# Kernel tuning notes

Measured on AMD Instinct MI355X. Metric: run time of the kernel, lower is better.

## Reference

```python
import jax, jax.numpy as jnp
import numpy as np

ALPHA_LO = float(np.exp(-1.0 / 5.0))   # 0.8187
ALPHA_HI = float(np.exp(-1.0 / 25.0))  # 0.9608
BN_EPS = 1e-5

B, T, D_IN, H = 32, 2000, 512, 512


def setup_inputs() -> dict:
    key = jax.random.key(0)
    ks = jax.random.split(key, 5)
    x = jax.random.normal(ks[0], (B, T, D_IN), dtype=jnp.float32)
    W = jax.random.normal(ks[1], (H, D_IN), dtype=jnp.float32) / np.sqrt(D_IN)
    b = jax.random.normal(ks[2], (H,), dtype=jnp.float32) * 0.01
    alpha = jax.random.uniform(ks[3], (H,), dtype=jnp.float32,
                               minval=ALPHA_LO, maxval=ALPHA_HI)
    gamma = jnp.ones((H,), dtype=jnp.float32)
    beta = jnp.zeros((H,), dtype=jnp.float32)
    ut0 = jax.random.uniform(ks[4], (B, H), dtype=jnp.float32)
    return {"x": x, "W": W, "b": b, "alpha": alpha,
            "gamma": gamma, "beta": beta, "ut0": ut0}


def reference(x, W, b, alpha, gamma, beta, ut0):
    # Linear: [B,T,Din] @ [Din,H] + b
    Wx = jnp.einsum("btd,hd->bth", x, W) + b
    # BatchNorm1d (training forward): stats over flattened (B*T) dim
    flat = Wx.reshape(-1, Wx.shape[-1])
    mean = flat.mean(axis=0)
    var = flat.var(axis=0)  # biased, as torch BN uses for normalization
    Wx = ((flat - mean) * jax.lax.rsqrt(var + BN_EPS) * gamma + beta).reshape(Wx.shape)
    # Readout cell: leaky integration + softmax accumulation over time
    a = jnp.clip(alpha, ALPHA_LO, ALPHA_HI)

    def step(carry, wxt):
        ut, acc = carry
        ut = a * ut + (1.0 - a) * wxt          # [B,H]
        acc = acc + jax.nn.softmax(ut, axis=1)
        return (ut, acc), None

    wx_t = jnp.transpose(Wx, (1, 0, 2))  # [T,B,H]
    (_, out), _ = jax.lax.scan(step, (ut0, jnp.zeros_like(ut0)), wx_t)
    return out[:, None, :]  # [B,1,H]
```

## Files before the change

### kernel.cpp

```cpp
#include <hip/hip_runtime.h>
#include <hip/hip_bf16.h>
#include <stdint.h>


namespace {
constexpr int kB = 32;
constexpr int kT = 2000;
constexpr int kD = 512;
constexpr int kH = 512;
constexpr int kM = kB * kT;
constexpr int kBM = 64;
constexpr int kNB = kM / kBM;
constexpr int kL = 16;
constexpr int kC = kT / kL;
constexpr int kG = 5;
constexpr int kNG = kC / kG;
constexpr float kALo = 0.81873075307798182f;
constexpr float kAHi = 0.96078943915232320f;

typedef __bf16 bf16x4 __attribute__((ext_vector_type(4)));
typedef __bf16 bf16x8 __attribute__((ext_vector_type(8)));
typedef float floatx16 __attribute__((ext_vector_type(16)));

__device__ __forceinline__ float bf2f(unsigned short u) {
  return __builtin_bit_cast(float, (unsigned)u << 16);
}
__device__ __forceinline__ float clipa(float a) {
  return fminf(fmaxf(a, kALo), kAHi);
}
__device__ __forceinline__ float pow16(float a) {
  const float a2 = a * a, a4 = a2 * a2, a8 = a4 * a4;
  return a8 * a8;
}

__global__ __launch_bounds__(256) void wcvt_k(const float* __restrict__ W,
                                              __bf16* __restrict__ Wbf,
                                              float* __restrict__ sums,
                                              float* __restrict__ out) {
  const int t = blockIdx.x * 256 + threadIdx.x;
  if (t < 2 * kH) sums[t] = 0.f;
  if (t < kB * kH) out[t] = 0.f;
  const float4 a0 = ((const float4*)W)[t * 2];
  const float4 a1 = ((const float4*)W)[t * 2 + 1];
  bf16x8 v;
  v[0] = (__bf16)a0.x; v[1] = (__bf16)a0.y; v[2] = (__bf16)a0.z; v[3] = (__bf16)a0.w;
  v[4] = (__bf16)a1.x; v[5] = (__bf16)a1.y; v[6] = (__bf16)a1.z; v[7] = (__bf16)a1.w;
  const int h = t >> 6, k8 = t & 63;
  *(bf16x8*)(Wbf + ((size_t)k8 * 512 + h) * 8) = v;
}

__global__ __launch_bounds__(512, 4) void gemm_k(const float* __restrict__ X,
                                                 const __bf16* __restrict__ Wbf,
                                                 const float* __restrict__ alpha,
                                                 unsigned short* __restrict__ Wxb,
                                                 float* __restrict__ vbuf,
                                                 float* __restrict__ partial) {
  __shared__ alignas(16) __bf16 As2[2][4][65][8];
  __shared__ float sred[2][kH];
  const int tid = threadIdx.x;
  const size_t row0 = (size_t)blockIdx.x * kBM;
  const int w = tid >> 6, L = tid & 63;
  const int ct0 = w * 2;
  const int lhalf = L >> 5, l32 = L & 31;
  const int arow = tid >> 3, acol = (tid & 7) * 4;
  const int akq = acol >> 3, aoff = acol & 7;

  floatx16 acc[2][2] = {};
  const float* xptr = X + (row0 + arow) * kD + acol;
  const __bf16* bptr = Wbf + ((size_t)(ct0 * 32) + l32) * 8;

  bf16x8 bE[4], bO[4];
  auto loadB = [&](bf16x8* dst, int s) {
#pragma unroll
    for (int kh = 0; kh < 2; ++kh) {
      const int kq = kh * 2 + lhalf;
      const __bf16* bq = bptr + (size_t)(s * 4 + kq) * 4096;
      dst[kh * 2 + 0] = *(const bf16x8*)bq;
      dst[kh * 2 + 1] = *(const bf16x8*)(bq + 256);
    }
  };
  auto stage = [&](int bufIdx, const float4& a) {
    bf16x4 av;
    av[0] = (__bf16)a.x; av[1] = (__bf16)a.y;
    av[2] = (__bf16)a.z; av[3] = (__bf16)a.w;
    *(bf16x4*)&As2[bufIdx][akq][arow][aoff] = av;
  };
  auto computeR = [&](int bufIdx, const bf16x8* bb) {
#pragma unroll
    for (int kh = 0; kh < 2; ++kh) {
      const int kq = kh * 2 + lhalf;
      const bf16x8 af0 = *(const bf16x8*)&As2[bufIdx][kq][l32][0];
      const bf16x8 af1 = *(const bf16x8*)&As2[bufIdx][kq][32 + l32][0];
      acc[0][0] = __builtin_amdgcn_mfma_f32_32x32x16_bf16(af0, bb[kh * 2 + 0], acc[0][0], 0, 0, 0);
      acc[0][1] = __builtin_amdgcn_mfma_f32_32x32x16_bf16(af0, bb[kh * 2 + 1], acc[0][1], 0, 0, 0);
      acc[1][0] = __builtin_amdgcn_mfma_f32_32x32x16_bf16(af1, bb[kh * 2 + 0], acc[1][0], 0, 0, 0);
      acc[1][1] = __builtin_amdgcn_mfma_f32_32x32x16_bf16(af1, bb[kh * 2 + 1], acc[1][1], 0, 0, 0);
    }
  };

  loadB(bE, 0);
  {
    const float4 a0 = *(const float4*)xptr;
    stage(0, a0);
  }
  float4 aA = *(const float4*)(xptr + 1 * 32);
  float4 aB = *(const float4*)(xptr + 2 * 32);
  asm volatile("s_waitcnt lgkmcnt(0)" ::: "memory");
  __builtin_amdgcn_s_barrier();

#pragma unroll 1
  for (int s = 0; s < 16; s += 2) {
    loadB(bO, s + 1);
    stage(1, aA);
    if (s + 3 < 16) aA = *(const float4*)(xptr + (s + 3) * 32);
    computeR(0, bE);
    asm volatile("s_waitcnt lgkmcnt(0)" ::: "memory");
    __builtin_amdgcn_s_barrier();
    const int o = s + 1;
    if (o < 15) {
      loadB(bE, o + 1);
      stage(0, aB);
      if (o + 3 < 16) aB = *(const float4*)(xptr + (o + 3) * 32);
    }
    computeR(1, bO);
    if (o < 15) {
      asm volatile("s_waitcnt lgkmcnt(0)" ::: "memory");
      __builtin_amdgcn_s_barrier();
    }
  }

  __syncthreads();
  sred[0][tid] = 0.f;
  sred[1][tid] = 0.f;
  __syncthreads();
#pragma unroll
  for (int c = 0; c < 2; ++c) {
    float s = 0.f, q = 0.f;
#pragma unroll
    for (int rt = 0; rt < 2; ++rt) {
#pragma unroll
      for (int r = 0; r < 16; ++r) {
        const float v = acc[rt][c][r];
        s += v;
        q += v * v;
      }
    }
    s += __shfl_xor(s, 32);
    q += __shfl_xor(q, 32);
    if (lhalf == 0) {
      atomicAdd(&sred[0][(ct0 + c) * 32 + l32], s);
      atomicAdd(&sred[1][(ct0 + c) * 32 + l32], q);
    }
  }

#pragma unroll
  for (int c = 0; c < 2; ++c) {
    const int col = (ct0 + c) * 32 + l32;
    const float a = clipa(alpha[col]);
    const float oma = 1.0f - a;
    const float a2 = a * a, a4 = a2 * a2, a8 = a4 * a4;
    float wgt[8];
    wgt[0] = a8 * a2 * a; wgt[1] = a8 * a2; wgt[2] = a8 * a; wgt[3] = a8;
    wgt[4] = a2 * a;      wgt[5] = a2;      wgt[6] = a;      wgt[7] = 1.0f;
    const float mult = (lhalf == 0) ? a4 * oma : oma;
#pragma unroll
    for (int j = 0; j < 8; ++j) wgt[j] *= mult;
#pragma unroll
    for (int rt = 0; rt < 2; ++rt) {
#pragma unroll
      for (int c32 = 0; c32 < 2; ++c32) {
        float S = 0.f;
#pragma unroll
        for (int j = 0; j < 8; ++j) S += wgt[j] * acc[rt][c][c32 * 8 + j];
        S += __shfl_xor(S, 32);
        if (lhalf == 0) {
          const int g = (int)blockIdx.x * 4 + rt * 2 + c32;
          vbuf[(size_t)g * kH + col] = S;
        }
      }
    }
  }

#pragma unroll
  for (int rt = 0; rt < 2; ++rt) {
#pragma unroll
    for (int c = 0; c < 2; ++c) {
      const int col = (ct0 + c) * 32 + l32;
#pragma unroll
      for (int r = 0; r < 16; ++r) {
        const int row = rt * 32 + 4 * lhalf + (r & 3) + 8 * (r >> 2);
        const unsigned short u = __builtin_bit_cast(unsigned short, (__bf16)acc[rt][c][r]);
        const unsigned un = __shfl_down((unsigned)u, 1);
        if ((l32 & 1) == 0)
          *(unsigned*)(Wxb + (row0 + row) * (size_t)kH + col) = (unsigned)u | (un << 16);
      }
    }
  }
  __syncthreads();
  partial[(size_t)blockIdx.x * 1024 + tid] = sred[0][tid];
  partial[(size_t)blockIdx.x * 1024 + 512 + tid] = sred[1][tid];
}

__global__ __launch_bounds__(512) void red1_k(const float* __restrict__ partial,
                                              float* __restrict__ sums) {
  const int tid = threadIdx.x;
  const int r0 = blockIdx.x * 25;
  float s0 = 0.f, s1 = 0.f;
#pragma unroll 5
  for (int r = 0; r < 25; ++r) {
    s0 += partial[(size_t)(r0 + r) * 1024 + tid];
    s1 += partial[(size_t)(r0 + r) * 1024 + 512 + tid];
  }
  atomicAdd(&sums[tid], s0);
  atomicAdd(&sums[kH + tid], s1);
}

__global__ __launch_bounds__(512) void fin_scan_k(const float* __restrict__ sums,
                                                  const float* __restrict__ alpha,
                                                  const float* __restrict__ gamma,
                                                  const float* __restrict__ beta,
                                                  const float* __restrict__ ut0,
                                                  float* __restrict__ prm,
                                                  const float* __restrict__ vbuf,
                                                  float* __restrict__ ustart) {
  const int h = threadIdx.x;
  const int b = blockIdx.x;
  const float inv_n = 1.0f / (float)kM;
  const float mean = sums[h] * inv_n;
  const float var = sums[kH + h] * inv_n - mean * mean;
  const float sc = gamma[h] * rsqrtf(var + 1e-5f);
  const float sh = beta[h] - mean * sc;
  const float a = clipa(alpha[h]);
  if (b == 0) {
    prm[h] = sc;
    prm[kH + h] = sh;
    prm[2 * kH + h] = a;
    prm[3 * kH + h] = 1.0f - a;
  }
  const float a16 = pow16(a);
  const float shc = sh * (1.0f - a16);
  float u = ut0[(size_t)b * kH + h];
  float vc[kG];
#pragma unroll 1
  for (int cb = 0; cb < kC; cb += kG) {
#pragma unroll
    for (int j = 0; j < kG; ++j)
      vc[j] = vbuf[((size_t)b * kC + cb + j) * kH + h];
    ustart[((size_t)b * kNG + cb / kG) * kH + h] = u;
#pragma unroll
    for (int j = 0; j < kG; ++j) u = a16 * u + sc * vc[j] + shc;
  }
}

__global__ __launch_bounds__(512) void soft_k(const unsigned short* __restrict__ Wxb,
                                              const float* __restrict__ prm,
                                              const float* __restrict__ ustart,
                                              float* __restrict__ out) {
  __shared__ float part[kL][9];
  __shared__ float zinv[kL];
  const int bc = blockIdx.x;
  const int b = bc / kNG, grp = bc % kNG;
  const int h = threadIdx.x;
  const int wv = h >> 6, lane = h & 63;
  const float sc = prm[h], sh = prm[kH + h];
  const float a = prm[2 * kH + h], oma = prm[3 * kH + h];
  float u = ustart[(size_t)bc * kH + h];
  const unsigned short* base =
      Wxb + ((size_t)b * kT + (size_t)grp * kG * kL) * kH + h;
  float acc = 0.f;
#pragma unroll 1
  for (int cc = 0; cc < kG; ++cc) {
    float e[kL];
#pragma unroll
    for (int i = 0; i < kL; ++i) {
      const float wvx = bf2f(base[(size_t)(cc * kL + i) * kH]) * sc + sh;
      u = a * u + oma * wvx;
      e[i] = __expf(u);
    }
#pragma unroll
    for (int i = 0; i < kL; ++i) {
      float s = e[i];
#pragma unroll
      for (int off = 32; off > 0; off >>= 1) s += __shfl_xor(s, off);
      if (lane == 0) part[i][wv] = s;
    }
    __syncthreads();
    if (h < kL) {
      float s = 0.f;
#pragma unroll
      for (int j = 0; j < 8; ++j) s += part[h][j];
      zinv[h] = 1.0f / s;
    }
    __syncthreads();
#pragma unroll
    for (int i = 0; i < kL; ++i) acc += e[i] * zinv[i];
    __syncthreads();
  }
  atomicAdd(&out[(size_t)b * kH + h], acc);
}

}

extern "C" void kernel_launch(void* const* d_in, const int* in_sizes, int n_in,
                              void* d_out, int out_size, void* d_ws, size_t ws_size,
                              hipStream_t stream) {
  const float* x = (const float*)d_in[0];
  const float* Wm = (const float*)d_in[1];
  const float* alpha = (const float*)d_in[3];
  const float* gamma = (const float*)d_in[4];
  const float* beta = (const float*)d_in[5];
  const float* ut0 = (const float*)d_in[6];
  float* out = (float*)d_out;

  float* wsp = (float*)d_ws;
  float* vbuf = wsp;
  float* ustart = vbuf + (size_t)kB * kC * kH;
  float* partial = ustart + (size_t)kB * kNG * kH;
  float* sums = partial + (size_t)1000 * 1024;
  float* prm = sums + 2 * kH;
  __bf16* Wbf = (__bf16*)(prm + 4 * kH);
  unsigned short* Wxb = (unsigned short*)(Wbf + (size_t)kH * kD);

  wcvt_k<<<128, 256, 0, stream>>>(Wm, Wbf, sums, out);
  gemm_k<<<kNB, 512, 0, stream>>>(x, Wbf, alpha, Wxb, vbuf, partial);
  red1_k<<<40, 512, 0, stream>>>(partial, sums);
  fin_scan_k<<<kB, 512, 0, stream>>>(sums, alpha, gamma, beta, ut0, prm, vbuf, ustart);
  soft_k<<<kB * kNG, 512, 0, stream>>>(Wxb, prm, ustart, out);
}
```

Baseline: 302.9 us.

## Load GEMM A operand directly from global into registers, drop LDS staging

The GEMM kernel no longer stages X tiles through shared memory with barriers. Each lane now loads its own MFMA A-fragment rows straight from global memory into registers, double-buffered, and converts them to bf16 in place. This removes the LDS writes, the LDS reads and the per-step barriers. In exchange every wave redundantly reads the same X rows (8 waves share the 64-row tile), and register use rises, so the occupancy hint is lowered from 4 to 2 blocks per CU.

Result: slower. 387.3 us (+27.9%).

```diff
diff --git a/kernel.cpp b/kernel.cpp
--- a/kernel.cpp
+++ b/kernel.cpp
@@ -49,27 +49,39 @@
   *(bf16x8*)(Wbf + ((size_t)k8 * 512 + h) * 8) = v;
 }
 
-__global__ __launch_bounds__(512, 4) void gemm_k(const float* __restrict__ X,
+__global__ __launch_bounds__(512, 2) void gemm_k(const float* __restrict__ X,
                                                  const __bf16* __restrict__ Wbf,
                                                  const float* __restrict__ alpha,
                                                  unsigned short* __restrict__ Wxb,
                                                  float* __restrict__ vbuf,
                                                  float* __restrict__ partial) {
-  __shared__ alignas(16) __bf16 As2[2][4][65][8];
   __shared__ float sred[2][kH];
   const int tid = threadIdx.x;
   const size_t row0 = (size_t)blockIdx.x * kBM;
   const int w = tid >> 6, L = tid & 63;
   const int ct0 = w * 2;
   const int lhalf = L >> 5, l32 = L & 31;
-  const int arow = tid >> 3, acol = (tid & 7) * 4;
-  const int akq = acol >> 3, aoff = acol & 7;
 
   floatx16 acc[2][2] = {};
-  const float* xptr = X + (row0 + arow) * kD + acol;
+  const float* xr0 = X + (row0 + l32) * kD + lhalf * 8;
+  const float* xr1 = X + (row0 + 32 + l32) * kD + lhalf * 8;
   const __bf16* bptr = Wbf + ((size_t)(ct0 * 32) + l32) * 8;
 
+  float4 aE[4][2], aO[4][2];
   bf16x8 bE[4], bO[4];
+
+  auto loadA = [&](float4 (*dst)[2], int s) {
+#pragma unroll
+    for (int rt = 0; rt < 2; ++rt) {
+      const float* xr = rt ? xr1 : xr0;
+#pragma unroll
+      for (int kh = 0; kh < 2; ++kh) {
+        const float* p = xr + s * 32 + kh * 16;
+        dst[rt * 2 + kh][0] = *(const float4*)p;
+        dst[rt * 2 + kh][1] = *(const float4*)(p + 4);
+      }
+    }
+  };
   auto loadB = [&](bf16x8* dst, int s) {
 #pragma unroll
     for (int kh = 0; kh < 2; ++kh) {
@@ -79,53 +91,47 @@
       dst[kh * 2 + 1] = *(const bf16x8*)(bq + 256);
     }
   };
-  auto stage = [&](int bufIdx, const float4& a) {
-    bf16x4 av;
-    av[0] = (__bf16)a.x; av[1] = (__bf16)a.y;
-    av[2] = (__bf16)a.z; av[3] = (__bf16)a.w;
-    *(bf16x4*)&As2[bufIdx][akq][arow][aoff] = av;
+  auto cvt8 = [](const float4 (&f)[2]) {
+    bf16x8 v;
+    v[0] = (__bf16)f[0].x; v[1] = (__bf16)f[0].y;
+    v[2] = (__bf16)f[0].z; v[3] = (__bf16)f[0].w;
+    v[4] = (__bf16)f[1].x; v[5] = (__bf16)f[1].y;
+    v[6] = (__bf16)f[1].z; v[7] = (__bf16)f[1].w;
+    return v;
   };
-  auto computeR = [&](int bufIdx, const bf16x8* bb) {
-#pragma unroll
-    for (int kh = 0; kh < 2; ++kh) {
-      const int kq = kh * 2 + lhalf;
-      const bf16x8 af0 = *(const bf16x8*)&As2[bufIdx][kq][l32][0];
-      const bf16x8 af1 = *(const bf16x8*)&As2[bufIdx][kq][32 + l32][0];
-      acc[0][0] = __builtin_amdgcn_mfma_f32_32x32x16_bf16(af0, bb[kh * 2 + 0], acc[0][0], 0, 0, 0);
-      acc[0][1] = __builtin_amdgcn_mfma_f32_32x32x16_bf16(af0, bb[kh * 2 + 1], acc[0][1], 0, 0, 0);
-      acc[1][0] = __builtin_amdgcn_mfma_f32_32x32x16_bf16(af1, bb[kh * 2 + 0], acc[1][0], 0, 0, 0);
-      acc[1][1] = __builtin_amdgcn_mfma_f32_32x32x16_bf16(af1, bb[kh * 2 + 1], acc[1][1], 0, 0, 0);
-    }
-  };
-
-  loadB(bE, 0);
-  {
-    const float4 a0 = *(const float4*)xptr;
-    stage(0, a0);
-  }
-  float4 aA = *(const float4*)(xptr + 1 * 32);
-  float4 aB = *(const float4*)(xptr + 2 * 32);
-  asm volatile("s_waitcnt lgkmcnt(0)" ::: "memory");
-  __builtin_amdgcn_s_barrier();
+
+  loadA(aE, 0); loadB(bE, 0);
+  loadA(aO, 1); loadB(bO, 1);
 
 #pragma unroll 1
   for (int s = 0; s < 16; s += 2) {
-    loadB(bO, s + 1);
-    stage(1, aA);
-    if (s + 3 < 16) aA = *(const float4*)(xptr + (s + 3) * 32);
-    computeR(0, bE);
-    asm volatile("s_waitcnt lgkmcnt(0)" ::: "memory");
-    __builtin_amdgcn_s_barrier();
-    const int o = s + 1;
-    if (o < 15) {
-      loadB(bE, o + 1);
-      stage(0, aB);
-      if (o + 3 < 16) aB = *(const float4*)(xptr + (o + 3) * 32);
-    }
-    computeR(1, bO);
-    if (o < 15) {
-      asm volatile("s_waitcnt lgkmcnt(0)" ::: "memory");
-      __builtin_amdgcn_s_barrier();
+    {
+      bf16x8 af[4];
+#pragma unroll
+      for (int f = 0; f < 4; ++f) af[f] = cvt8(aE[f]);
+      if (s + 2 < 16) loadA(aE, s + 2);
+#pragma unroll
+      for (int kh = 0; kh < 2; ++kh) {
+        acc[0][0] = __builtin_amdgcn_mfma_f32_32x32x16_bf16(af[kh], bE[kh * 2 + 0], acc[0][0], 0, 0, 0);
+        acc[0][1] = __builtin_amdgcn_mfma_f32_32x32x16_bf16(af[kh], bE[kh * 2 + 1], acc[0][1], 0, 0, 0);
+        acc[1][0] = __builtin_amdgcn_mfma_f32_32x32x16_bf16(af[2 + kh], bE[kh * 2 + 0], acc[1][0], 0, 0, 0);
+        acc[1][1] = __builtin_amdgcn_mfma_f32_32x32x16_bf16(af[2 + kh], bE[kh * 2 + 1], acc[1][1], 0, 0, 0);
+      }
+      if (s + 2 < 16) loadB(bE, s + 2);
+    }
+    {
+      bf16x8 af[4];
+#pragma unroll
+      for (int f = 0; f < 4; ++f) af[f] = cvt8(aO[f]);
+      if (s + 3 < 16) loadA(aO, s + 3);
+#pragma unroll
+      for (int kh = 0; kh < 2; ++kh) {
+        acc[0][0] = __builtin_amdgcn_mfma_f32_32x32x16_bf16(af[kh], bO[kh * 2 + 0], acc[0][0], 0, 0, 0);
+        acc[0][1] = __builtin_amdgcn_mfma_f32_32x32x16_bf16(af[kh], bO[kh * 2 + 1], acc[0][1], 0, 0, 0);
+        acc[1][0] = __builtin_amdgcn_mfma_f32_32x32x16_bf16(af[2 + kh], bO[kh * 2 + 0], acc[1][0], 0, 0, 0);
+        acc[1][1] = __builtin_amdgcn_mfma_f32_32x32x16_bf16(af[2 + kh], bO[kh * 2 + 1], acc[1][1], 0, 0, 0);
+      }
+      if (s + 3 < 16) loadB(bO, s + 3);
     }
   }
 
```

## Restructure softmax pass to one wave per 16-step chunk with in-wave reductions

Applied to the files above, without the earlier changes.

The scan kernel now writes the carried state at every 16-step chunk boundary in place into vbuf, instead of every 80 steps into a separate ustart buffer. The softmax kernel assigns one 64-lane wave per (batch, chunk), with each lane covering 8 hidden units loaded as a vector. The softmax normalizer is therefore a pure wave shuffle reduction with no shared memory or block barriers, and the grid grows to 1000 blocks for more parallelism. The GEMM block index is also swizzled so neighbouring blocks cover distant row tiles, which changes L2/channel access patterns. Per-element atomics to out increase in number.

Result: slower. 332.2 us (+9.7%).

```diff
diff --git a/kernel.cpp b/kernel.cpp
--- a/kernel.cpp
+++ b/kernel.cpp
@@ -14,12 +14,12 @@
 constexpr int kL = 16;
 constexpr int kC = kT / kL;
 constexpr int kG = 5;
-constexpr int kNG = kC / kG;
 constexpr float kALo = 0.81873075307798182f;
 constexpr float kAHi = 0.96078943915232320f;
 
 typedef __bf16 bf16x4 __attribute__((ext_vector_type(4)));
 typedef __bf16 bf16x8 __attribute__((ext_vector_type(8)));
+typedef unsigned short u16x8 __attribute__((ext_vector_type(8)));
 typedef float floatx16 __attribute__((ext_vector_type(16)));
 
 __device__ __forceinline__ float bf2f(unsigned short u) {
@@ -58,7 +58,8 @@
   __shared__ alignas(16) __bf16 As2[2][4][65][8];
   __shared__ float sred[2][kH];
   const int tid = threadIdx.x;
-  const size_t row0 = (size_t)blockIdx.x * kBM;
+  const int swz = (blockIdx.x & 7) * (kNB / 8) + (blockIdx.x >> 3);
+  const size_t row0 = (size_t)swz * kBM;
   const int w = tid >> 6, L = tid & 63;
   const int ct0 = w * 2;
   const int lhalf = L >> 5, l32 = L & 31;
@@ -174,7 +175,7 @@
         for (int j = 0; j < 8; ++j) S += wgt[j] * acc[rt][c][c32 * 8 + j];
         S += __shfl_xor(S, 32);
         if (lhalf == 0) {
-          const int g = (int)blockIdx.x * 4 + rt * 2 + c32;
+          const int g = swz * 4 + rt * 2 + c32;
           vbuf[(size_t)g * kH + col] = S;
         }
       }
@@ -221,8 +222,7 @@
                                                   const float* __restrict__ beta,
                                                   const float* __restrict__ ut0,
                                                   float* __restrict__ prm,
-                                                  const float* __restrict__ vbuf,
-                                                  float* __restrict__ ustart) {
+                                                  float* __restrict__ vbuf) {
   const int h = threadIdx.x;
   const int b = blockIdx.x;
   const float inv_n = 1.0f / (float)kM;
@@ -246,57 +246,61 @@
 #pragma unroll
     for (int j = 0; j < kG; ++j)
       vc[j] = vbuf[((size_t)b * kC + cb + j) * kH + h];
-    ustart[((size_t)b * kNG + cb / kG) * kH + h] = u;
-#pragma unroll
-    for (int j = 0; j < kG; ++j) u = a16 * u + sc * vc[j] + shc;
-  }
-}
-
-__global__ __launch_bounds__(512) void soft_k(const unsigned short* __restrict__ Wxb,
-                                              const float* __restrict__ prm,
-                                              const float* __restrict__ ustart,
-                                              float* __restrict__ out) {
-  __shared__ float part[kL][9];
-  __shared__ float zinv[kL];
-  const int bc = blockIdx.x;
-  const int b = bc / kNG, grp = bc % kNG;
-  const int h = threadIdx.x;
-  const int wv = h >> 6, lane = h & 63;
-  const float sc = prm[h], sh = prm[kH + h];
-  const float a = prm[2 * kH + h], oma = prm[3 * kH + h];
-  float u = ustart[(size_t)bc * kH + h];
-  const unsigned short* base =
-      Wxb + ((size_t)b * kT + (size_t)grp * kG * kL) * kH + h;
-  float acc = 0.f;
-#pragma unroll 1
-  for (int cc = 0; cc < kG; ++cc) {
-    float e[kL];
-#pragma unroll
-    for (int i = 0; i < kL; ++i) {
-      const float wvx = bf2f(base[(size_t)(cc * kL + i) * kH]) * sc + sh;
-      u = a * u + oma * wvx;
-      e[i] = __expf(u);
-    }
-#pragma unroll
-    for (int i = 0; i < kL; ++i) {
-      float s = e[i];
-#pragma unroll
-      for (int off = 32; off > 0; off >>= 1) s += __shfl_xor(s, off);
-      if (lane == 0) part[i][wv] = s;
-    }
-    __syncthreads();
-    if (h < kL) {
-      float s = 0.f;
-#pragma unroll
-      for (int j = 0; j < 8; ++j) s += part[h][j];
-      zinv[h] = 1.0f / s;
-    }
-    __syncthreads();
-#pragma unroll
-    for (int i = 0; i < kL; ++i) acc += e[i] * zinv[i];
-    __syncthreads();
-  }
-  atomicAdd(&out[(size_t)b * kH + h], acc);
+#pragma unroll
+    for (int j = 0; j < kG; ++j) {
+      vbuf[((size_t)b * kC + cb + j) * kH + h] = u;
+      u = a16 * u + sc * vc[j] + shc;
+    }
+  }
+}
+
+__global__ __launch_bounds__(256, 4) void soft_k(const unsigned short* __restrict__ Wxb,
+                                                 const float* __restrict__ prm,
+                                                 const float* __restrict__ ustart,
+                                                 float* __restrict__ out) {
+  const int tid = threadIdx.x;
+  const int wv = tid >> 6, lane = tid & 63;
+  const int unit = blockIdx.x * 4 + wv;
+  const int b = unit / kC, c = unit % kC;
+  const int h0 = lane * 8;
+
+  float sc[8], sh[8], av[8], om[8], u[8], acc[8];
+  *(float4*)&sc[0] = *(const float4*)(prm + h0);
+  *(float4*)&sc[4] = *(const float4*)(prm + h0 + 4);
+  *(float4*)&sh[0] = *(const float4*)(prm + kH + h0);
+  *(float4*)&sh[4] = *(const float4*)(prm + kH + h0 + 4);
+  *(float4*)&av[0] = *(const float4*)(prm + 2 * kH + h0);
+  *(float4*)&av[4] = *(const float4*)(prm + 2 * kH + h0 + 4);
+  *(float4*)&om[0] = *(const float4*)(prm + 3 * kH + h0);
+  *(float4*)&om[4] = *(const float4*)(prm + 3 * kH + h0 + 4);
+  const float* up = ustart + ((size_t)b * kC + c) * kH + h0;
+  *(float4*)&u[0] = *(const float4*)up;
+  *(float4*)&u[4] = *(const float4*)(up + 4);
+#pragma unroll
+  for (int j = 0; j < 8; ++j) acc[j] = 0.f;
+
+  const unsigned short* base = Wxb + ((size_t)b * kT + (size_t)c * kL) * kH + h0;
+#pragma unroll
+  for (int i = 0; i < kL; ++i) {
+    const u16x8 v = *(const u16x8*)(base + (size_t)i * kH);
+    float e[8];
+    float ls = 0.f;
+#pragma unroll
+    for (int j = 0; j < 8; ++j) {
+      const float wvx = bf2f(v[j]) * sc[j] + sh[j];
+      u[j] = av[j] * u[j] + om[j] * wvx;
+      e[j] = __expf(u[j]);
+      ls += e[j];
+    }
+#pragma unroll
+    for (int off = 32; off > 0; off >>= 1) ls += __shfl_xor(ls, off);
+    const float zi = 1.0f / ls;
+#pragma unroll
+    for (int j = 0; j < 8; ++j) acc[j] += e[j] * zi;
+  }
+#pragma unroll
+  for (int j = 0; j < 8; ++j)
+    atomicAdd(&out[(size_t)b * kH + h0 + j], acc[j]);
 }
 
 }
@@ -314,8 +318,7 @@
 
   float* wsp = (float*)d_ws;
   float* vbuf = wsp;
-  float* ustart = vbuf + (size_t)kB * kC * kH;
-  float* partial = ustart + (size_t)kB * kNG * kH;
+  float* partial = vbuf + (size_t)kB * kC * kH;
   float* sums = partial + (size_t)1000 * 1024;
   float* prm = sums + 2 * kH;
   __bf16* Wbf = (__bf16*)(prm + 4 * kH);
@@ -324,6 +327,6 @@
   wcvt_k<<<128, 256, 0, stream>>>(Wm, Wbf, sums, out);
   gemm_k<<<kNB, 512, 0, stream>>>(x, Wbf, alpha, Wxb, vbuf, partial);
   red1_k<<<40, 512, 0, stream>>>(partial, sums);
-  fin_scan_k<<<kB, 512, 0, stream>>>(sums, alpha, gamma, beta, ut0, prm, vbuf, ustart);
-  soft_k<<<kB * kNG, 512, 0, stream>>>(Wxb, prm, ustart, out);
-}
+  fin_scan_k<<<kB, 512, 0, stream>>>(sums, alpha, gamma, beta, ut0, prm, vbuf);
+  soft_k<<<1000, 256, 0, stream>>>(Wxb, prm, vbuf, out);
+}
```
